# Performance work log

Measured on AMD Instinct MI355X. Metric: run time of the kernel, lower is better.

## Reference

```python
import jax, jax.numpy as jnp
import numpy as np

B, U, V = 4, 64, 256
IN_DIM, STATE_DIM, CODE_DIM = 768, 768, 384
NUM_HEADS, HEAD_DIM = 8, 64
INNER = NUM_HEADS * HEAD_DIM  # 512
SCALE = HEAD_DIM ** 0.5


def _ln(x, g, b, eps=1e-5):
    mu = jnp.mean(x, axis=-1, keepdims=True)
    var = jnp.var(x, axis=-1, keepdims=True)
    return (x - mu) * jax.lax.rsqrt(var + eps) * g + b


def setup_inputs() -> dict:
    key = jax.random.key(0)
    ks = jax.random.split(key, 12)
    def w(k, shape, s=0.02):
        return jax.random.normal(k, shape, jnp.float32) * s
    return {
        "receiver_states": jax.random.normal(ks[0], (B, U, STATE_DIM), jnp.float32),
        "receiver_codes": jax.random.normal(ks[1], (B, U, CODE_DIM), jnp.float32),
        "sender_states": jax.random.normal(ks[2], (B, V, IN_DIM), jnp.float32),
        "ln_r_g": jnp.ones((STATE_DIM,), jnp.float32),
        "ln_r_b": jnp.zeros((STATE_DIM,), jnp.float32),
        "ln_s_g": jnp.ones((IN_DIM,), jnp.float32),
        "ln_s_b": jnp.zeros((IN_DIM,), jnp.float32),
        "Wq": w(ks[3], (STATE_DIM, INNER)), "bq": jnp.zeros((INNER,), jnp.float32), "Wmq": w(ks[4], (CODE_DIM, STATE_DIM)),
        "Wk": w(ks[5], (IN_DIM, INNER)),   "bk": jnp.zeros((INNER,), jnp.float32), "Wmk": w(ks[6], (CODE_DIM, IN_DIM)),
        "Wv": w(ks[7], (IN_DIM, INNER)),   "bv": jnp.zeros((INNER,), jnp.float32), "Wmv": w(ks[8], (CODE_DIM, IN_DIM)),
        "We": w(ks[9], (INNER, STATE_DIM)), "be": jnp.zeros((STATE_DIM,), jnp.float32), "Wme": w(ks[10], (CODE_DIM, INNER)),
        "gamma": jnp.ones((STATE_DIM,), jnp.float32),  # LayerScale, init 1.0
    }


def reference(receiver_states, receiver_codes, sender_states,
              ln_r_g, ln_r_b, ln_s_g, ln_s_b,
              Wq, bq, Wmq, Wk, bk, Wmk, Wv, bv, Wmv, We, be, Wme, gamma):
    r = _ln(receiver_states, ln_r_g, ln_r_b)   # (b,u,ds)
    s = _ln(sender_states, ln_s_g, ln_s_b)     # (b,v,di)
    # ModFC: y = (x * (1 + ctx @ Wm)) @ W + b  (code-conditioned input modulation)
    q = (r * (1.0 + receiver_codes @ Wmq)) @ Wq + bq          # (b,u,inner)
    mk = 1.0 + receiver_codes @ Wmk                           # (b,u,di)
    mv = 1.0 + receiver_codes @ Wmv                           # (b,u,di)
    xs = s[:, :, None, :]                                     # (b,v,1,di)
    k = (xs * mk[:, None, :, :]) @ Wk + bk                    # (b,v,u,inner)
    v = (xs * mv[:, None, :, :]) @ Wv + bv                    # (b,v,u,inner)
    qh = q.reshape(B, U, NUM_HEADS, HEAD_DIM)
    kh = k.reshape(B, V, U, NUM_HEADS, HEAD_DIM)
    vh = v.reshape(B, V, U, NUM_HEADS, HEAD_DIM)
    scores = jnp.einsum('buhc,bvuhc->bhuv', qh, kh) / SCALE   # (b,h,u,v)
    weights = jax.nn.softmax(scores, axis=-1)
    msg = jnp.einsum('bhuv,bvuhc->buhc', weights, vh).reshape(B, U, INNER)
    out = (msg * (1.0 + receiver_codes @ Wme)) @ We + be      # exit ModFC -> (b,u,ds)
    out = out * gamma                                         # LayerScale
    return receiver_states + out                              # residual
```

## Files before the change

### kernel.cpp

```cpp
#include <hip/hip_runtime.h>


#define DD 768
#define CDIM 384
#define NH 8
#define HD 64
#define INNER 512
#define VV 256

__device__ __forceinline__ void fma4(float4& a, float s, const float4& b) {
  a.x += s * b.x; a.y += s * b.y; a.z += s * b.z; a.w += s * b.w;
}

template <int K, int NS>
__device__ __forceinline__ void gcore(const float* __restrict__ A0, int lda,
                                      const float* __restrict__ Bp,
                                      float4& a0, float4& a1, float4& a2,
                                      float4& a3) {
  float4 b0[8], b1[8];
#pragma unroll
  for (int i = 0; i < 8; i++) b0[i] = *(const float4*)(Bp + (size_t)i * NS);
  const float* Bq = Bp + (size_t)8 * NS;
#pragma unroll 1
  for (int kk = 0; kk < K; kk += 16) {
#pragma unroll
    for (int i = 0; i < 8; i++) b1[i] = *(const float4*)(Bq + (size_t)i * NS);
    Bq += (size_t)8 * NS;
#pragma unroll
    for (int i = 0; i < 8; i++) {
      float4 bv = b0[i]; int k = kk + i;
      fma4(a0, A0[k], bv); fma4(a1, A0[lda + k], bv);
      fma4(a2, A0[2 * lda + k], bv); fma4(a3, A0[3 * lda + k], bv);
    }
    if (kk + 16 < K) {
#pragma unroll
      for (int i = 0; i < 8; i++) b0[i] = *(const float4*)(Bq + (size_t)i * NS);
      Bq += (size_t)8 * NS;
    }
#pragma unroll
    for (int i = 0; i < 8; i++) {
      float4 bv = b1[i]; int k = kk + 8 + i;
      fma4(a0, A0[k], bv); fma4(a1, A0[lda + k], bv);
      fma4(a2, A0[2 * lda + k], bv); fma4(a3, A0[3 * lda + k], bv);
    }
  }
}

__global__ __launch_bounds__(256, 2) void k_s1(
    const float* __restrict__ ss, const float* __restrict__ rs,
    const float* __restrict__ g_s, const float* __restrict__ b_s,
    const float* __restrict__ g_r, const float* __restrict__ b_r,
    const float* __restrict__ codes, const float* __restrict__ Wmq,
    const float* __restrict__ Wmk, const float* __restrict__ Wmv,
    const float* __restrict__ Wme, const float* __restrict__ Wk,
    float* __restrict__ s_ln, float* __restrict__ r_ln,
    float* __restrict__ cp, float* __restrict__ WkT) {
  __shared__ float SB[6144];
  int bid = blockIdx.x, t = threadIdx.x;
  if (bid < 176) {
    int nc = bid % 11, mb = bid / 11;
    int base = nc * 256;
    const float* W; int N, colW;
    if (base < 768)       { W = Wmq; N = DD;    colW = base; }
    else if (base < 1536) { W = Wmk; N = DD;    colW = base - 768; }
    else if (base < 2304) { W = Wmv; N = DD;    colW = base - 1536; }
    else                  { W = Wme; N = INNER; colW = base - 2304; }
    int m0 = mb * 16;
#pragma unroll
    for (int p = 0; p < 24; p++) {
      int idx = p * 256 + t, r = idx / 384, k = idx % 384;
      SB[idx] = codes[(size_t)(m0 + r) * CDIM + k];
    }
    __syncthreads();
    int kl = t & 63, wid = t >> 6;
    const float* A0 = SB + (wid * 4) * 384;
    float4 a0 = {0,0,0,0}, a1 = {0,0,0,0}, a2 = {0,0,0,0}, a3 = {0,0,0,0};
    if (N == DD)
      gcore<384, DD>(A0, 384, W + colW + 4 * kl, a0, a1, a2, a3);
    else
      gcore<384, INNER>(A0, 384, W + colW + 4 * kl, a0, a1, a2, a3);
    int m = m0 + wid * 4, gcol = base + 4 * kl;
    *(float4*)(cp + (size_t)m * 2816 + gcol) = a0;
    *(float4*)(cp + (size_t)(m + 1) * 2816 + gcol) = a1;
    *(float4*)(cp + (size_t)(m + 2) * 2816 + gcol) = a2;
    *(float4*)(cp + (size_t)(m + 3) * 2816 + gcol) = a3;
  } else if (bid < 272) {
    int tid = bid - 176;
    int d0 = (tid >> 3) * 64, c0 = (tid & 7) * 64;
    int j = t & 63, i0 = t >> 6;
#pragma unroll
    for (int p = 0; p < 16; p++) {
      int i = p * 4 + i0;
      SB[i * 65 + j] = Wk[(size_t)(d0 + i) * INNER + c0 + j];
    }
    __syncthreads();
#pragma unroll
    for (int p = 0; p < 16; p++) {
      int i = p * 4 + i0;
      WkT[(size_t)(c0 + i) * DD + d0 + j] = SB[j * 65 + i];
    }
  } else {
    int rr = bid - 272;
    const float *x, *g, *bb; float* y; int r;
    if (rr < 1024) { x = ss; g = g_s; bb = b_s; y = s_ln; r = rr; }
    else           { x = rs; g = g_r; bb = b_r; y = r_ln; r = rr - 1024; }
    const float* xr = x + (size_t)r * DD;
    float v0 = xr[t], v1 = xr[t + 256], v2 = xr[t + 512];
    float s = v0 + v1 + v2, sq = v0 * v0 + v1 * v1 + v2 * v2;
    for (int o = 32; o > 0; o >>= 1) {
      s += __shfl_down(s, o, 64); sq += __shfl_down(sq, o, 64);
    }
    int wid = t >> 6, lane = t & 63;
    if (lane == 0) { SB[wid] = s; SB[wid + 4] = sq; }
    __syncthreads();
    float sum = SB[0] + SB[1] + SB[2] + SB[3];
    float ssq = SB[4] + SB[5] + SB[6] + SB[7];
    float mu = sum * (1.0f / 768.0f);
    float var = ssq * (1.0f / 768.0f) - mu * mu;
    float rstd = rsqrtf(var + 1e-5f);
    float* yr = y + (size_t)r * DD;
    yr[t]       = (v0 - mu) * rstd * g[t]       + bb[t];
    yr[t + 256] = (v1 - mu) * rstd * g[t + 256] + bb[t + 256];
    yr[t + 512] = (v2 - mu) * rstd * g[t + 512] + bb[t + 512];
  }
}

__global__ __launch_bounds__(256, 2) void k_s2(
    const float* __restrict__ s_ln, const float* __restrict__ r_ln,
    const float* __restrict__ cp, const float* __restrict__ Wq,
    float* __restrict__ sT, float* __restrict__ qp) {
  __shared__ float SB[4160];
  int bid = blockIdx.x, t = threadIdx.x;
  if (bid < 128) {
    int ks = bid & 3, tile = bid >> 2, nc = tile & 1, mb = tile >> 1;
    int m0 = mb * 16, col0 = nc * 256, k0 = ks * 192;
#pragma unroll
    for (int p = 0; p < 12; p++) {
      int idx = p * 256 + t, r = idx / 192, k = idx % 192;
      int d = k0 + k;
      float mqv = cp[(size_t)(m0 + r) * 2816 + d] + 1.0f;
      SB[idx] = r_ln[(size_t)(m0 + r) * DD + d] * mqv;
    }
    __syncthreads();
    int kl = t & 63, wid = t >> 6;
    int col = col0 + 4 * kl;
    const float* A0 = SB + (wid * 4) * 192;
    float4 a0 = {0,0,0,0}, a1 = {0,0,0,0}, a2 = {0,0,0,0}, a3 = {0,0,0,0};
    gcore<192, INNER>(A0, 192, Wq + (size_t)k0 * INNER + col, a0, a1, a2, a3);
    int m = m0 + wid * 4;
    float* dst = qp + (size_t)ks * (256 * INNER);
    *(float4*)(dst + (size_t)m * INNER + col) = a0;
    *(float4*)(dst + (size_t)(m + 1) * INNER + col) = a1;
    *(float4*)(dst + (size_t)(m + 2) * INNER + col) = a2;
    *(float4*)(dst + (size_t)(m + 3) * INNER + col) = a3;
  } else {
    int tid = bid - 128;
    int vt = tid & 3, dt = (tid >> 2) % 12, b = tid / 48;
    int v0 = vt * 64, d0 = dt * 64;
    int j = t & 63, i0 = t >> 6;
#pragma unroll
    for (int p = 0; p < 16; p++) {
      int i = p * 4 + i0;
      SB[i * 65 + j] = s_ln[(size_t)(b * VV + v0 + i) * DD + d0 + j];
    }
    __syncthreads();
#pragma unroll
    for (int p = 0; p < 16; p++) {
      int i = p * 4 + i0;
      sT[((size_t)b * DD + d0 + i) * VV + v0 + j] = SB[j * 65 + i];
    }
  }
}

__global__ __launch_bounds__(256, 2) void k_s3(
    const float* __restrict__ qp, const float* __restrict__ bq,
    const float* __restrict__ WkT, const float* __restrict__ cp,
    const float* __restrict__ bk, float* __restrict__ qm,
    float* __restrict__ qbk) {
  __shared__ float SB[1024];
  int bid = blockIdx.x, t = threadIdx.x;
  if (bid < 384) {
    int h = bid & 7, dc = (bid >> 3) % 3, mb = bid / 24;
    int m0 = mb * 16;
#pragma unroll
    for (int p = 0; p < 4; p++) {
      int idx = p * 256 + t, r = idx >> 6, c = idx & 63;
      int i = h * HD + c;
      size_t off = (size_t)(m0 + r) * INNER + i;
      SB[idx] = qp[off] + qp[131072 + off] + qp[262144 + off] +
                qp[393216 + off] + bq[i];
    }
    __syncthreads();
    int kl = t & 63, wid = t >> 6;
    int col = dc * 256 + 4 * kl;
    const float* A0 = SB + (wid * 4) * HD;
    float4 a0 = {0,0,0,0}, a1 = {0,0,0,0}, a2 = {0,0,0,0}, a3 = {0,0,0,0};
    gcore<64, DD>(A0, HD, WkT + (size_t)(h * HD) * DD + col, a0, a1, a2, a3);
#pragma unroll
    for (int j = 0; j < 4; j++) {
      float4 a = (j == 0) ? a0 : (j == 1) ? a1 : (j == 2) ? a2 : a3;
      int m = m0 + wid * 4 + j;
      const float* mkp = cp + (size_t)m * 2816 + 768 + col;
      float4 o = {a.x * (mkp[0] + 1.0f), a.y * (mkp[1] + 1.0f),
                  a.z * (mkp[2] + 1.0f), a.w * (mkp[3] + 1.0f)};
      *(float4*)(qm + ((size_t)m * NH + h) * DD + col) = o;
    }
  } else {
    int m = bid - 384;
    size_t off = (size_t)m * INNER;
    SB[t] = (qp[off + t] + qp[131072 + off + t] + qp[262144 + off + t] +
             qp[393216 + off + t] + bq[t]) * bk[t];
    int t2 = t + 256;
    SB[t2] = (qp[off + t2] + qp[131072 + off + t2] + qp[262144 + off + t2] +
              qp[393216 + off + t2] + bq[t2]) * bk[t2];
    __syncthreads();
    if (t < 8) {
      float a = 0.f;
      for (int c = 0; c < HD; c++) a += SB[t * HD + c];
      qbk[m * NH + t] = a;
    }
  }
}

__global__ __launch_bounds__(256, 2) void k_s4(
    const float* __restrict__ qm, const float* __restrict__ sT,
    float* __restrict__ scp) {
  __shared__ float SB[3072];
  int bid = blockIdx.x, t = threadIdx.x;
  int ks = bid & 3, b = (bid >> 2) & 3, mb = bid >> 4;
  int gi0 = b * 512 + mb * 16, k0 = ks * 192;
#pragma unroll
  for (int p = 0; p < 12; p++) {
    int idx = p * 256 + t, r = idx / 192, k = idx % 192;
    SB[idx] = qm[(size_t)(gi0 + r) * DD + k0 + k];
  }
  __syncthreads();
  int kl = t & 63, wid = t >> 6;
  int col = 4 * kl;
  const float* A0 = SB + (wid * 4) * 192;
  float4 a0 = {0,0,0,0}, a1 = {0,0,0,0}, a2 = {0,0,0,0}, a3 = {0,0,0,0};
  gcore<192, VV>(A0, 192, sT + ((size_t)b * DD + k0) * VV + col, a0, a1, a2, a3);
  int gi = gi0 + wid * 4;
  float* dst = scp + (size_t)ks * (2048 * VV);
  *(float4*)(dst + (size_t)gi * VV + col) = a0;
  *(float4*)(dst + (size_t)(gi + 1) * VV + col) = a1;
  *(float4*)(dst + (size_t)(gi + 2) * VV + col) = a2;
  *(float4*)(dst + (size_t)(gi + 3) * VV + col) = a3;
}

__global__ __launch_bounds__(256, 2) void k_s5(
    const float* __restrict__ scp, const float* __restrict__ qbk,
    const float* __restrict__ s_ln, const float* __restrict__ cp,
    float* __restrict__ wsm) {
  __shared__ float SC[4096];
  int bid = blockIdx.x, t = threadIdx.x;
  int dc = bid % 3, up = (bid / 3) % 32, b = bid / 96;
  int gi0 = b * 512 + up * 16;
#pragma unroll
  for (int p = 0; p < 16; p++) {
    int idx = p * 256 + t, r = idx >> 8, c = idx & 255;
    size_t o = (size_t)(gi0 + r) * VV + c;
    float v = scp[o] + scp[524288 + o] + scp[1048576 + o] + scp[1572864 + o];
    int m = b * 64 + up * 2 + (r >> 3), h = r & 7;
    SC[idx] = (v + qbk[m * NH + h]) * 0.125f;
  }
  __syncthreads();
  int wid = t >> 6, lane = t & 63;
#pragma unroll
  for (int j = 0; j < 4; j++) {
    int r = wid * 4 + j;
    float x0 = SC[r * 256 + lane],       x1 = SC[r * 256 + lane + 64];
    float x2 = SC[r * 256 + lane + 128], x3 = SC[r * 256 + lane + 192];
    float mx = fmaxf(fmaxf(x0, x1), fmaxf(x2, x3));
    for (int o = 1; o < 64; o <<= 1) mx = fmaxf(mx, __shfl_xor(mx, o, 64));
    float e0 = __expf(x0 - mx), e1 = __expf(x1 - mx);
    float e2 = __expf(x2 - mx), e3 = __expf(x3 - mx);
    float sm = e0 + e1 + e2 + e3;
    for (int o = 1; o < 64; o <<= 1) sm += __shfl_xor(sm, o, 64);
    float rinv = 1.0f / sm;
    SC[r * 256 + lane] = e0 * rinv;       SC[r * 256 + lane + 64] = e1 * rinv;
    SC[r * 256 + lane + 128] = e2 * rinv; SC[r * 256 + lane + 192] = e3 * rinv;
  }
  __syncthreads();
  int kl = t & 63;
  int col = dc * 256 + 4 * kl;
  const float* A0 = SC + (wid * 4) * 256;
  float4 a0 = {0,0,0,0}, a1 = {0,0,0,0}, a2 = {0,0,0,0}, a3 = {0,0,0,0};
  gcore<VV, DD>(A0, 256, s_ln + (size_t)(b * VV) * DD + col, a0, a1, a2, a3);
#pragma unroll
  for (int j = 0; j < 4; j++) {
    float4 a = (j == 0) ? a0 : (j == 1) ? a1 : (j == 2) ? a2 : a3;
    int r = wid * 4 + j;
    int ul = r >> 3, h = r & 7, m = b * 64 + up * 2 + ul;
    const float* mvp = cp + (size_t)m * 2816 + 1536 + col;
    float4 o = {a.x * (mvp[0] + 1.0f), a.y * (mvp[1] + 1.0f),
                a.z * (mvp[2] + 1.0f), a.w * (mvp[3] + 1.0f)};
    *(float4*)(wsm + ((size_t)h * 256 + m) * DD + col) = o;
  }
}

__global__ __launch_bounds__(256, 2) void k_s6(
    const float* __restrict__ wsm, const float* __restrict__ Wv,
    float* __restrict__ mmp) {
  __shared__ float AL[6144];
  int bid = blockIdx.x, t = threadIdx.x;
  int hp = bid & 1, ks = (bid >> 1) & 7, mb = bid >> 4;
  int h0 = hp * 4, m0 = mb * 16, k0 = ks * 96;
#pragma unroll
  for (int p = 0; p < 24; p++) {
    int idx = p * 256 + t;
    int e = idx / 1536, rem = idx % 1536, r = rem / 96, k = rem % 96;
    AL[idx] = wsm[((size_t)(h0 + e) * 256 + m0 + r) * DD + k0 + k];
  }
  __syncthreads();
  int kl = t & 63, wid = t >> 6;
  int hs = kl >> 4, c4 = 4 * (kl & 15);
  int colg = h0 * HD + hs * HD + c4;
  const float* A0 = AL + (hs * 16 + wid * 4) * 96;
  float4 a0 = {0,0,0,0}, a1 = {0,0,0,0}, a2 = {0,0,0,0}, a3 = {0,0,0,0};
  gcore<96, INNER>(A0, 96, Wv + (size_t)k0 * INNER + colg, a0, a1, a2, a3);
  float* dst = mmp + (size_t)ks * (256 * INNER);
  int m = m0 + wid * 4;
  *(float4*)(dst + (size_t)m * INNER + colg) = a0;
  *(float4*)(dst + (size_t)(m + 1) * INNER + colg) = a1;
  *(float4*)(dst + (size_t)(m + 2) * INNER + colg) = a2;
  *(float4*)(dst + (size_t)(m + 3) * INNER + colg) = a3;
}

__global__ __launch_bounds__(256, 2) void k_s7(
    const float* __restrict__ mmp, const float* __restrict__ bvv,
    const float* __restrict__ cp, const float* __restrict__ We,
    float* __restrict__ op) {
  __shared__ float AL[1024];
  int bid = blockIdx.x, t = threadIdx.x;
  int ks = bid & 7, dc = (bid >> 3) % 3, mb = bid / 24;
  int m0 = mb * 16, k0 = ks * 64;
#pragma unroll
  for (int p = 0; p < 4; p++) {
    int idx = p * 256 + t, r = idx >> 6, k = idx & 63;
    int i = k0 + k;
    size_t off = (size_t)(m0 + r) * INNER + i;
    float v = mmp[off] + mmp[131072 + off] + mmp[262144 + off] +
              mmp[393216 + off] + mmp[524288 + off] + mmp[655360 + off] +
              mmp[786432 + off] + mmp[917504 + off];
    float mev = cp[(size_t)(m0 + r) * 2816 + 2304 + i] + 1.0f;
    AL[idx] = (v + bvv[i]) * mev;
  }
  __syncthreads();
  int kl = t & 63, wid = t >> 6;
  int col = dc * 256 + 4 * kl;
  const float* A0 = AL + (wid * 4) * 64;
  float4 a0 = {0,0,0,0}, a1 = {0,0,0,0}, a2 = {0,0,0,0}, a3 = {0,0,0,0};
  gcore<64, DD>(A0, 64, We + (size_t)k0 * DD + col, a0, a1, a2, a3);
  float* dst = op + (size_t)ks * (256 * DD);
  int m = m0 + wid * 4;
  *(float4*)(dst + (size_t)m * DD + col) = a0;
  *(float4*)(dst + (size_t)(m + 1) * DD + col) = a1;
  *(float4*)(dst + (size_t)(m + 2) * DD + col) = a2;
  *(float4*)(dst + (size_t)(m + 3) * DD + col) = a3;
}

__global__ __launch_bounds__(256) void k_s8(
    const float* __restrict__ op, const float* __restrict__ be,
    const float* __restrict__ gamma, const float* __restrict__ rs,
    float* __restrict__ outp) {
  int m = blockIdx.x, t = threadIdx.x;
#pragma unroll
  for (int j = 0; j < 3; j++) {
    int d = t + j * 256;
    size_t off = (size_t)m * DD + d;
    float v = op[off] + op[196608 + off] + op[393216 + off] +
              op[589824 + off] + op[786432 + off] + op[983040 + off] +
              op[1179648 + off] + op[1376256 + off];
    outp[off] = rs[off] + (v + be[d]) * gamma[d];
  }
}

extern "C" void kernel_launch(void* const* d_in, const int* in_sizes, int n_in,
                              void* d_out, int out_size, void* d_ws, size_t ws_size,
                              hipStream_t stream) {
  const float* rs     = (const float*)d_in[0];
  const float* codes  = (const float*)d_in[1];
  const float* ss     = (const float*)d_in[2];
  const float* ln_r_g = (const float*)d_in[3];
  const float* ln_r_b = (const float*)d_in[4];
  const float* ln_s_g = (const float*)d_in[5];
  const float* ln_s_b = (const float*)d_in[6];
  const float* Wq  = (const float*)d_in[7];
  const float* bq  = (const float*)d_in[8];
  const float* Wk  = (const float*)d_in[10];
  const float* bk  = (const float*)d_in[11];
  const float* Wmq = (const float*)d_in[9];
  const float* Wmk = (const float*)d_in[12];
  const float* Wv  = (const float*)d_in[13];
  const float* bv  = (const float*)d_in[14];
  const float* Wmv = (const float*)d_in[15];
  const float* We  = (const float*)d_in[16];
  const float* be  = (const float*)d_in[17];
  const float* Wme = (const float*)d_in[18];
  const float* gamma = (const float*)d_in[19];

  float* w = (float*)d_ws;
  float* s_ln = w;
  float* r_ln = w + 786432;
  float* WkT  = w + 983040;
  float* qp   = w + 1376256;
  float* sT   = w + 1900544;
  float* cp   = w + 2686976;
  float* qbk  = w + 3407872;
  float* qm   = w + 3409920;
  float* scp  = w + 4982784;
  float* wsm  = qm;
  float* mmp  = r_ln;
  float* op   = scp;

  k_s1<<<dim3(1552), 256, 0, stream>>>(ss, rs, ln_s_g, ln_s_b, ln_r_g, ln_r_b,
                                       codes, Wmq, Wmk, Wmv, Wme, Wk,
                                       s_ln, r_ln, cp, WkT);
  k_s2<<<dim3(320), 256, 0, stream>>>(s_ln, r_ln, cp, Wq, sT, qp);
  k_s3<<<dim3(640), 256, 0, stream>>>(qp, bq, WkT, cp, bk, qm, qbk);
  k_s4<<<dim3(512), 256, 0, stream>>>(qm, sT, scp);
  k_s5<<<dim3(384), 256, 0, stream>>>(scp, qbk, s_ln, cp, wsm);
  k_s6<<<dim3(256), 256, 0, stream>>>(wsm, Wv, mmp);
  k_s7<<<dim3(384), 256, 0, stream>>>(mmp, bv, cp, We, op);
  k_s8<<<dim3(256), 256, 0, stream>>>(op, be, gamma, rs, (float*)d_out);
}
```

Before: 198.9 us.

## Split GEMM K dimension across waves with LDS cross-wave reduction

Each wave now computes all 16 rows of the tile over a quarter of the K range instead of 4 rows over the full K, so every B (weight) float4 loaded from global memory is reused across 16 rows rather than 4. This cuts global weight traffic per block about fourfold and uses vectorized float4 LDS reads for A. Partial sums are combined through a shared-memory reduction with two extra barriers. In exchange each thread holds 16 float4 accumulators, raising register pressure, and LDS allocation grows to 48KB per block, which may limit occupancy.

Result: slower. 297.1 us (+49.3%).

```diff
diff --git a/kernel.cpp b/kernel.cpp
--- a/kernel.cpp
+++ b/kernel.cpp
@@ -12,36 +12,88 @@
   a.x += s * b.x; a.y += s * b.y; a.z += s * b.z; a.w += s * b.w;
 }
 
-template <int K, int NS>
-__device__ __forceinline__ void gcore(const float* __restrict__ A0, int lda,
-                                      const float* __restrict__ Bp,
-                                      float4& a0, float4& a1, float4& a2,
-                                      float4& a3) {
+__device__ __forceinline__ void fma_chunk(const float* __restrict__ Aw, int lda,
+                                          int kk, const float4* b,
+                                          float4* acc) {
+#pragma unroll
+  for (int rg = 0; rg < 4; rg++) {
+    const float* ap = Aw + (rg * 4) * lda + kk;
+    float4 a0l = *(const float4*)(ap);
+    float4 a0h = *(const float4*)(ap + 4);
+    float4 a1l = *(const float4*)(ap + lda);
+    float4 a1h = *(const float4*)(ap + lda + 4);
+    float4 a2l = *(const float4*)(ap + 2 * lda);
+    float4 a2h = *(const float4*)(ap + 2 * lda + 4);
+    float4 a3l = *(const float4*)(ap + 3 * lda);
+    float4 a3h = *(const float4*)(ap + 3 * lda + 4);
+    float4* ac = acc + rg * 4;
+    fma4(ac[0], a0l.x, b[0]); fma4(ac[1], a1l.x, b[0]);
+    fma4(ac[2], a2l.x, b[0]); fma4(ac[3], a3l.x, b[0]);
+    fma4(ac[0], a0l.y, b[1]); fma4(ac[1], a1l.y, b[1]);
+    fma4(ac[2], a2l.y, b[1]); fma4(ac[3], a3l.y, b[1]);
+    fma4(ac[0], a0l.z, b[2]); fma4(ac[1], a1l.z, b[2]);
+    fma4(ac[2], a2l.z, b[2]); fma4(ac[3], a3l.z, b[2]);
+    fma4(ac[0], a0l.w, b[3]); fma4(ac[1], a1l.w, b[3]);
+    fma4(ac[2], a2l.w, b[3]); fma4(ac[3], a3l.w, b[3]);
+    fma4(ac[0], a0h.x, b[4]); fma4(ac[1], a1h.x, b[4]);
+    fma4(ac[2], a2h.x, b[4]); fma4(ac[3], a3h.x, b[4]);
+    fma4(ac[0], a0h.y, b[5]); fma4(ac[1], a1h.y, b[5]);
+    fma4(ac[2], a2h.y, b[5]); fma4(ac[3], a3h.y, b[5]);
+    fma4(ac[0], a0h.z, b[6]); fma4(ac[1], a1h.z, b[6]);
+    fma4(ac[2], a2h.z, b[6]); fma4(ac[3], a3h.z, b[6]);
+    fma4(ac[0], a0h.w, b[7]); fma4(ac[1], a1h.w, b[7]);
+    fma4(ac[2], a2h.w, b[7]); fma4(ac[3], a3h.w, b[7]);
+  }
+}
+
+template <int KQ, int NS>
+__device__ __forceinline__ void gcore16(const float* __restrict__ Aw, int lda,
+                                        const float* __restrict__ Bp,
+                                        float4* acc) {
   float4 b0[8], b1[8];
-#pragma unroll
-  for (int i = 0; i < 8; i++) b0[i] = *(const float4*)(Bp + (size_t)i * NS);
-  const float* Bq = Bp + (size_t)8 * NS;
+  const float* Bq = Bp;
+#pragma unroll
+  for (int i = 0; i < 8; i++) b0[i] = *(const float4*)(Bq + (size_t)i * NS);
+  Bq += (size_t)8 * NS;
 #pragma unroll 1
-  for (int kk = 0; kk < K; kk += 16) {
+  for (int kk = 0; kk + 16 <= KQ; kk += 16) {
 #pragma unroll
     for (int i = 0; i < 8; i++) b1[i] = *(const float4*)(Bq + (size_t)i * NS);
     Bq += (size_t)8 * NS;
-#pragma unroll
-    for (int i = 0; i < 8; i++) {
-      float4 bv = b0[i]; int k = kk + i;
-      fma4(a0, A0[k], bv); fma4(a1, A0[lda + k], bv);
-      fma4(a2, A0[2 * lda + k], bv); fma4(a3, A0[3 * lda + k], bv);
-    }
-    if (kk + 16 < K) {
+    fma_chunk(Aw, lda, kk, b0, acc);
+    if (kk + 16 < KQ) {
 #pragma unroll
       for (int i = 0; i < 8; i++) b0[i] = *(const float4*)(Bq + (size_t)i * NS);
       Bq += (size_t)8 * NS;
     }
-#pragma unroll
-    for (int i = 0; i < 8; i++) {
-      float4 bv = b1[i]; int k = kk + 8 + i;
-      fma4(a0, A0[k], bv); fma4(a1, A0[lda + k], bv);
-      fma4(a2, A0[2 * lda + k], bv); fma4(a3, A0[3 * lda + k], bv);
+    fma_chunk(Aw, lda, kk + 8, b1, acc);
+  }
+  if (KQ % 16 == 8) fma_chunk(Aw, lda, (KQ / 16) * 16, b0, acc);
+}
+
+__device__ __forceinline__ void wave_reduce(const float4* acc, float4* fin,
+                                            float* RED, int wid, int kl) {
+  __syncthreads();
+  float4* R4 = (float4*)RED;
+#pragma unroll
+  for (int r = 0; r < 16; r++) {
+    int rg = r >> 2;
+    if (rg != wid) {
+      int r12 = r - (rg > wid ? 4 : 0);
+      R4[(wid * 12 + r12) * 64 + kl] = acc[r];
+    }
+    if (rg == wid) fin[r & 3] = acc[r];
+  }
+  __syncthreads();
+#pragma unroll
+  for (int j = 0; j < 4; j++) {
+    int r = wid * 4 + j;
+#pragma unroll
+    for (int w = 0; w < 4; w++) {
+      if (w == wid) continue;
+      int r12 = r - (wid > w ? 4 : 0);
+      float4 v = R4[(w * 12 + r12) * 64 + kl];
+      fin[j].x += v.x; fin[j].y += v.y; fin[j].z += v.z; fin[j].w += v.w;
     }
   }
 }
@@ -55,7 +107,7 @@
     const float* __restrict__ Wme, const float* __restrict__ Wk,
     float* __restrict__ s_ln, float* __restrict__ r_ln,
     float* __restrict__ cp, float* __restrict__ WkT) {
-  __shared__ float SB[6144];
+  __shared__ float SB[12288];
   int bid = blockIdx.x, t = threadIdx.x;
   if (bid < 176) {
     int nc = bid % 11, mb = bid / 11;
@@ -73,17 +125,18 @@
     }
     __syncthreads();
     int kl = t & 63, wid = t >> 6;
-    const float* A0 = SB + (wid * 4) * 384;
-    float4 a0 = {0,0,0,0}, a1 = {0,0,0,0}, a2 = {0,0,0,0}, a3 = {0,0,0,0};
+    float4 acc[16] = {};
+    const float* Aw = SB + wid * 96;
     if (N == DD)
-      gcore<384, DD>(A0, 384, W + colW + 4 * kl, a0, a1, a2, a3);
+      gcore16<96, DD>(Aw, 384, W + (size_t)(wid * 96) * DD + colW + 4 * kl, acc);
     else
-      gcore<384, INNER>(A0, 384, W + colW + 4 * kl, a0, a1, a2, a3);
+      gcore16<96, INNER>(Aw, 384, W + (size_t)(wid * 96) * INNER + colW + 4 * kl, acc);
+    float4 fin[4];
+    wave_reduce(acc, fin, SB, wid, kl);
     int m = m0 + wid * 4, gcol = base + 4 * kl;
-    *(float4*)(cp + (size_t)m * 2816 + gcol) = a0;
-    *(float4*)(cp + (size_t)(m + 1) * 2816 + gcol) = a1;
-    *(float4*)(cp + (size_t)(m + 2) * 2816 + gcol) = a2;
-    *(float4*)(cp + (size_t)(m + 3) * 2816 + gcol) = a3;
+#pragma unroll
+    for (int j = 0; j < 4; j++)
+      *(float4*)(cp + (size_t)(m + j) * 2816 + gcol) = fin[j];
   } else if (bid < 272) {
     int tid = bid - 176;
     int d0 = (tid >> 3) * 64, c0 = (tid & 7) * 64;
@@ -129,7 +182,7 @@
     const float* __restrict__ s_ln, const float* __restrict__ r_ln,
     const float* __restrict__ cp, const float* __restrict__ Wq,
     float* __restrict__ sT, float* __restrict__ qp) {
-  __shared__ float SB[4160];
+  __shared__ float SB[12288];
   int bid = blockIdx.x, t = threadIdx.x;
   if (bid < 128) {
     int ks = bid & 3, tile = bid >> 2, nc = tile & 1, mb = tile >> 1;
@@ -144,15 +197,16 @@
     __syncthreads();
     int kl = t & 63, wid = t >> 6;
     int col = col0 + 4 * kl;
-    const float* A0 = SB + (wid * 4) * 192;
-    float4 a0 = {0,0,0,0}, a1 = {0,0,0,0}, a2 = {0,0,0,0}, a3 = {0,0,0,0};
-    gcore<192, INNER>(A0, 192, Wq + (size_t)k0 * INNER + col, a0, a1, a2, a3);
+    float4 acc[16] = {};
+    gcore16<48, INNER>(SB + wid * 48, 192,
+                       Wq + (size_t)(k0 + wid * 48) * INNER + col, acc);
+    float4 fin[4];
+    wave_reduce(acc, fin, SB, wid, kl);
     int m = m0 + wid * 4;
     float* dst = qp + (size_t)ks * (256 * INNER);
-    *(float4*)(dst + (size_t)m * INNER + col) = a0;
-    *(float4*)(dst + (size_t)(m + 1) * INNER + col) = a1;
-    *(float4*)(dst + (size_t)(m + 2) * INNER + col) = a2;
-    *(float4*)(dst + (size_t)(m + 3) * INNER + col) = a3;
+#pragma unroll
+    for (int j = 0; j < 4; j++)
+      *(float4*)(dst + (size_t)(m + j) * INNER + col) = fin[j];
   } else {
     int tid = bid - 128;
     int vt = tid & 3, dt = (tid >> 2) % 12, b = tid / 48;
@@ -177,7 +231,7 @@
     const float* __restrict__ WkT, const float* __restrict__ cp,
     const float* __restrict__ bk, float* __restrict__ qm,
     float* __restrict__ qbk) {
-  __shared__ float SB[1024];
+  __shared__ float SB[12288];
   int bid = blockIdx.x, t = threadIdx.x;
   if (bid < 384) {
     int h = bid & 7, dc = (bid >> 3) % 3, mb = bid / 24;
@@ -193,16 +247,17 @@
     __syncthreads();
     int kl = t & 63, wid = t >> 6;
     int col = dc * 256 + 4 * kl;
-    const float* A0 = SB + (wid * 4) * HD;
-    float4 a0 = {0,0,0,0}, a1 = {0,0,0,0}, a2 = {0,0,0,0}, a3 = {0,0,0,0};
-    gcore<64, DD>(A0, HD, WkT + (size_t)(h * HD) * DD + col, a0, a1, a2, a3);
+    float4 acc[16] = {};
+    gcore16<16, DD>(SB + wid * 16, HD,
+                    WkT + (size_t)(h * HD + wid * 16) * DD + col, acc);
+    float4 fin[4];
+    wave_reduce(acc, fin, SB, wid, kl);
 #pragma unroll
     for (int j = 0; j < 4; j++) {
-      float4 a = (j == 0) ? a0 : (j == 1) ? a1 : (j == 2) ? a2 : a3;
       int m = m0 + wid * 4 + j;
       const float* mkp = cp + (size_t)m * 2816 + 768 + col;
-      float4 o = {a.x * (mkp[0] + 1.0f), a.y * (mkp[1] + 1.0f),
-                  a.z * (mkp[2] + 1.0f), a.w * (mkp[3] + 1.0f)};
+      float4 o = {fin[j].x * (mkp[0] + 1.0f), fin[j].y * (mkp[1] + 1.0f),
+                  fin[j].z * (mkp[2] + 1.0f), fin[j].w * (mkp[3] + 1.0f)};
       *(float4*)(qm + ((size_t)m * NH + h) * DD + col) = o;
     }
   } else {
@@ -225,7 +280,7 @@
 __global__ __launch_bounds__(256, 2) void k_s4(
     const float* __restrict__ qm, const float* __restrict__ sT,
     float* __restrict__ scp) {
-  __shared__ float SB[3072];
+  __shared__ float SB[12288];
   int bid = blockIdx.x, t = threadIdx.x;
   int ks = bid & 3, b = (bid >> 2) & 3, mb = bid >> 4;
   int gi0 = b * 512 + mb * 16, k0 = ks * 192;
@@ -237,22 +292,23 @@
   __syncthreads();
   int kl = t & 63, wid = t >> 6;
   int col = 4 * kl;
-  const float* A0 = SB + (wid * 4) * 192;
-  float4 a0 = {0,0,0,0}, a1 = {0,0,0,0}, a2 = {0,0,0,0}, a3 = {0,0,0,0};
-  gcore<192, VV>(A0, 192, sT + ((size_t)b * DD + k0) * VV + col, a0, a1, a2, a3);
+  float4 acc[16] = {};
+  gcore16<48, VV>(SB + wid * 48, 192,
+                  sT + ((size_t)b * DD + k0 + wid * 48) * VV + col, acc);
+  float4 fin[4];
+  wave_reduce(acc, fin, SB, wid, kl);
   int gi = gi0 + wid * 4;
   float* dst = scp + (size_t)ks * (2048 * VV);
-  *(float4*)(dst + (size_t)gi * VV + col) = a0;
-  *(float4*)(dst + (size_t)(gi + 1) * VV + col) = a1;
-  *(float4*)(dst + (size_t)(gi + 2) * VV + col) = a2;
-  *(float4*)(dst + (size_t)(gi + 3) * VV + col) = a3;
+#pragma unroll
+  for (int j = 0; j < 4; j++)
+    *(float4*)(dst + (size_t)(gi + j) * VV + col) = fin[j];
 }
 
 __global__ __launch_bounds__(256, 2) void k_s5(
     const float* __restrict__ scp, const float* __restrict__ qbk,
     const float* __restrict__ s_ln, const float* __restrict__ cp,
     float* __restrict__ wsm) {
-  __shared__ float SC[4096];
+  __shared__ float SC[12288];
   int bid = blockIdx.x, t = threadIdx.x;
   int dc = bid % 3, up = (bid / 3) % 32, b = bid / 96;
   int gi0 = b * 512 + up * 16;
@@ -284,17 +340,18 @@
   __syncthreads();
   int kl = t & 63;
   int col = dc * 256 + 4 * kl;
-  const float* A0 = SC + (wid * 4) * 256;
-  float4 a0 = {0,0,0,0}, a1 = {0,0,0,0}, a2 = {0,0,0,0}, a3 = {0,0,0,0};
-  gcore<VV, DD>(A0, 256, s_ln + (size_t)(b * VV) * DD + col, a0, a1, a2, a3);
+  float4 acc[16] = {};
+  gcore16<64, DD>(SC + wid * 64, 256,
+                  s_ln + (size_t)(b * VV + wid * 64) * DD + col, acc);
+  float4 fin[4];
+  wave_reduce(acc, fin, SC, wid, kl);
 #pragma unroll
   for (int j = 0; j < 4; j++) {
-    float4 a = (j == 0) ? a0 : (j == 1) ? a1 : (j == 2) ? a2 : a3;
     int r = wid * 4 + j;
     int ul = r >> 3, h = r & 7, m = b * 64 + up * 2 + ul;
     const float* mvp = cp + (size_t)m * 2816 + 1536 + col;
-    float4 o = {a.x * (mvp[0] + 1.0f), a.y * (mvp[1] + 1.0f),
-                a.z * (mvp[2] + 1.0f), a.w * (mvp[3] + 1.0f)};
+    float4 o = {fin[j].x * (mvp[0] + 1.0f), fin[j].y * (mvp[1] + 1.0f),
+                fin[j].z * (mvp[2] + 1.0f), fin[j].w * (mvp[3] + 1.0f)};
     *(float4*)(wsm + ((size_t)h * 256 + m) * DD + col) = o;
   }
 }
@@ -302,7 +359,7 @@
 __global__ __launch_bounds__(256, 2) void k_s6(
     const float* __restrict__ wsm, const float* __restrict__ Wv,
     float* __restrict__ mmp) {
-  __shared__ float AL[6144];
+  __shared__ float AL[12288];
   int bid = blockIdx.x, t = threadIdx.x;
   int hp = bid & 1, ks = (bid >> 1) & 7, mb = bid >> 4;
   int h0 = hp * 4, m0 = mb * 16, k0 = ks * 96;
@@ -316,22 +373,23 @@
   int kl = t & 63, wid = t >> 6;
   int hs = kl >> 4, c4 = 4 * (kl & 15);
   int colg = h0 * HD + hs * HD + c4;
-  const float* A0 = AL + (hs * 16 + wid * 4) * 96;
-  float4 a0 = {0,0,0,0}, a1 = {0,0,0,0}, a2 = {0,0,0,0}, a3 = {0,0,0,0};
-  gcore<96, INNER>(A0, 96, Wv + (size_t)k0 * INNER + colg, a0, a1, a2, a3);
+  const float* Aw = AL + hs * 1536 + wid * 24;
+  float4 acc[16] = {};
+  gcore16<24, INNER>(Aw, 96, Wv + (size_t)(k0 + wid * 24) * INNER + colg, acc);
+  float4 fin[4];
+  wave_reduce(acc, fin, AL, wid, kl);
   float* dst = mmp + (size_t)ks * (256 * INNER);
   int m = m0 + wid * 4;
-  *(float4*)(dst + (size_t)m * INNER + colg) = a0;
-  *(float4*)(dst + (size_t)(m + 1) * INNER + colg) = a1;
-  *(float4*)(dst + (size_t)(m + 2) * INNER + colg) = a2;
-  *(float4*)(dst + (size_t)(m + 3) * INNER + colg) = a3;
+#pragma unroll
+  for (int j = 0; j < 4; j++)
+    *(float4*)(dst + (size_t)(m + j) * INNER + colg) = fin[j];
 }
 
 __global__ __launch_bounds__(256, 2) void k_s7(
     const float* __restrict__ mmp, const float* __restrict__ bvv,
     const float* __restrict__ cp, const float* __restrict__ We,
     float* __restrict__ op) {
-  __shared__ float AL[1024];
+  __shared__ float AL[12288];
   int bid = blockIdx.x, t = threadIdx.x;
   int ks = bid & 7, dc = (bid >> 3) % 3, mb = bid / 24;
   int m0 = mb * 16, k0 = ks * 64;
@@ -349,15 +407,16 @@
   __syncthreads();
   int kl = t & 63, wid = t >> 6;
   int col = dc * 256 + 4 * kl;
-  const float* A0 = AL + (wid * 4) * 64;
-  float4 a0 = {0,0,0,0}, a1 = {0,0,0,0}, a2 = {0,0,0,0}, a3 = {0,0,0,0};
-  gcore<64, DD>(A0, 64, We + (size_t)k0 * DD + col, a0, a1, a2, a3);
+  float4 acc[16] = {};
+  gcore16<16, DD>(AL + wid * 16, 64,
+                  We + (size_t)(k0 + wid * 16) * DD + col, acc);
+  float4 fin[4];
+  wave_reduce(acc, fin, AL, wid, kl);
   float* dst = op + (size_t)ks * (256 * DD);
   int m = m0 + wid * 4;
-  *(float4*)(dst + (size_t)m * DD + col) = a0;
-  *(float4*)(dst + (size_t)(m + 1) * DD + col) = a1;
-  *(float4*)(dst + (size_t)(m + 2) * DD + col) = a2;
-  *(float4*)(dst + (size_t)(m + 3) * DD + col) = a3;
+#pragma unroll
+  for (int j = 0; j < 4; j++)
+    *(float4*)(dst + (size_t)(m + j) * DD + col) = fin[j];
 }
 
 __global__ __launch_bounds__(256) void k_s8(
```
